# Kernel tuning notes

Measured on AMD Instinct MI355X. Metric: run time of the kernel, lower is better.

Reference implementation:

```python
import jax, jax.numpy as jnp
import numpy as np

I, H, M, C, LOC, K = 512, 256, 80, 1024, 32, 31
C2 = C // 2
B, S, T = 32, 256, 800


def setup_inputs() -> dict:
    key = jax.random.key(0)
    ks = jax.random.split(key, 20)
    sc = 0.02
    return {
        "encodings": jax.random.normal(ks[0], (B, S, I), jnp.float32),
        "queries": jax.random.normal(ks[1], (B, T, H), jnp.float32),
        "outputs": jax.random.normal(ks[2], (B, T, M), jnp.float32),
        "mask": jnp.ones((B, S), jnp.float32),
        # GRUCell (PyTorch layout: gates ordered r, z, n)
        "w_ih": jax.random.normal(ks[3], (3 * C, I + H), jnp.float32) * sc,
        "w_hh": jax.random.normal(ks[4], (3 * C, C), jnp.float32) * sc,
        "b_ih": jax.random.normal(ks[5], (3 * C,), jnp.float32) * sc,
        "b_hh": jax.random.normal(ks[6], (3 * C,), jnp.float32) * sc,
        "w_q": jax.random.normal(ks[7], (C2, C), jnp.float32) * sc,        # proj_query
        "w_loc1": jax.random.normal(ks[8], (LOC, 1, K), jnp.float32) * sc, # Conv1d(1, loc, K)
        "w_loc2": jax.random.normal(ks[9], (C2, LOC), jnp.float32) * sc,   # Conv1d(loc, C2, 1)
        "w_k": jax.random.normal(ks[10], (C2, I), jnp.float32) * sc,       # proj_key
        "b_k": jax.random.normal(ks[11], (C2,), jnp.float32) * sc,
        "w_agg": jax.random.normal(ks[12], (C2,), jnp.float32) * sc,       # Conv1d(C2, 1, 1)
        "w_t1": jax.random.normal(ks[13], (C, I + C + M), jnp.float32) * sc,
        "b_t1": jax.random.normal(ks[14], (C,), jnp.float32) * sc,
        "w_t2": jax.random.normal(ks[15], (C,), jnp.float32) * sc,
    }


def _conv1d(x, w, pad):
    # x: [B, Cin, S], w: [Cout, Cin, K]
    return jax.lax.conv_general_dilated(
        x, w, window_strides=(1,), padding=[(pad, pad)],
        dimension_numbers=("NCH", "OIH", "NCH"))


def _aligner(encodings, queries, outputs, maskb,
             w_ih, w_hh, b_ih, b_hh, w_q, w_loc1, w_loc2, w_k, b_k,
             w_agg, w_t1, b_t1, w_t2):
    bsize, seqlen, _ = encodings.shape
    # key projection: [B, S, C2]
    key = encodings @ w_k.T + b_k
    h0 = jnp.zeros((bsize, C), encodings.dtype)
    align0 = jnp.full((bsize, seqlen), 1.0 / seqlen, encodings.dtype)
    alpha0 = jnp.zeros((bsize, seqlen), encodings.dtype).at[:, 0].set(1.0)
    trans0 = jnp.full((bsize, 1), 0.5, encodings.dtype)

    def step(carry, xt):
        h, align, trans, alpha = carry
        query, frame = xt  # [B,H], [B,M]
        prev = jnp.einsum("bsi,bs->bi", encodings, alpha)
        x = jnp.concatenate([query, prev], axis=-1)  # [B, H+I]
        gx = x @ w_ih.T + b_ih
        gh = h @ w_hh.T + b_hh
        xr, xz, xn = jnp.split(gx, 3, axis=-1)
        hr, hz, hn = jnp.split(gh, 3, axis=-1)
        r = jax.nn.sigmoid(xr + hr)
        z = jax.nn.sigmoid(xz + hz)
        n = jnp.tanh(xn + r * hn)
        h_new = (1.0 - z) * n + z * h  # GRUCell update
        # location features: [B,1,S] -> [B,LOC,S] -> [B,C2,S]
        loc = _conv1d(align[:, None, :], w_loc1, K // 2)
        loc = jnp.einsum("cl,bls->bcs", w_loc2, loc)
        score = loc + (h_new @ w_q.T)[..., None] + key.swapaxes(1, 2)  # [B,C2,S]
        energy = jnp.einsum("c,bcs->bs", w_agg, jnp.tanh(score))
        energy = jnp.where(maskb, -jnp.inf, energy)
        align_new = jax.nn.softmax(energy, axis=-1)
        shifted = jnp.pad(alpha, ((0, 0), (1, 0)))[:, :-1]  # F.pad(alpha, [1,-1])
        alpha_new = ((1.0 - trans) * alpha + trans * shifted + 1e-7) * align_new
        alpha_new = alpha_new / alpha_new.sum(axis=-1, keepdims=True)
        attend = jnp.einsum("bsi,bs->bi", encodings, alpha_new)
        t_in = jnp.concatenate([attend, frame, h_new], axis=-1)
        t = jax.nn.sigmoid(jnp.tanh(t_in @ w_t1.T + b_t1) @ w_t2[:, None])  # [B,1]
        return (h_new, align_new, t, alpha_new), alpha_new

    xs = (queries.swapaxes(0, 1), outputs.swapaxes(0, 1))
    _, alphas = jax.lax.scan(step, (h0, align0, trans0, alpha0), xs)
    return alphas.swapaxes(0, 1)  # [B, T, S]


def reference(encodings, queries, outputs, mask,
              w_ih, w_hh, b_ih, b_hh, w_q, w_loc1, w_loc2, w_k, b_k,
              w_agg, w_t1, b_t1, w_t2):
    maskb = ~(mask.astype(bool))
    return _aligner(encodings, queries, outputs, maskb,
                    w_ih, w_hh, b_ih, b_hh, w_q, w_loc1, w_loc2, w_k, b_k,
                    w_agg, w_t1, b_t1, w_t2)
```

## Files before the change

### kernel.cpp

```cpp
#include <hip/hip_runtime.h>
#include <cstdint>
#include <cstddef>


namespace cfg {
constexpr int NB = 32, NS = 256, NI = 512, NHq = 256, NM = 80;
constexpr int NC = 1024, NC2 = 512, NT = 800;
constexpr int NBLK = 256, NTHR = 512;

constexpr size_t OFF_KEYT  = 0;
constexpr size_t OFF_WKT   = OFF_KEYT + (size_t)NB * NS * NC2;
constexpr size_t OFF_PU    = OFF_WKT + (size_t)NI * NC2;
constexpr size_t OFF_H     = OFF_PU + (size_t)2 * NB * NI;
constexpr size_t OFF_H16   = OFF_H + (size_t)2 * NC * NB;
constexpr size_t OFF_E     = OFF_H16 + (size_t)NB * NC;
constexpr size_t OFF_W     = OFF_E + (size_t)2 * NB * NS;
constexpr size_t OFF_SE    = OFF_W + (size_t)2 * NB * NS;
constexpr size_t OFF_SW    = OFF_SE + 64;
constexpr size_t OFF_TPART = OFF_SW + 64;
constexpr size_t OFF_TRED  = OFF_TPART + (size_t)NBLK * NB;
constexpr size_t OFF_QBUF  = OFF_TRED + 32;
constexpr size_t OFF_BAR   = OFF_QBUF + (size_t)NB * NC2;
constexpr size_t OFF_Q16   = OFF_BAR + 4608;
constexpr size_t OFF_F16   = OFF_Q16 + (size_t)NT * NB * NHq / 2;
constexpr size_t OFF_WQ16  = OFF_F16 + (size_t)NT * NB * 128 / 2;
constexpr size_t WS_FLOATS = OFF_WQ16 + (size_t)NC2 * NC / 2;
}
using namespace cfg;

typedef __attribute__((ext_vector_type(8))) short short8;
typedef __attribute__((ext_vector_type(4))) float f32x4;

#define MF(a, b, c) __builtin_amdgcn_mfma_f32_16x16x32_bf16((a), (b), (c), 0, 0, 0)
#define LDSC(d, p) asm volatile("global_load_dwordx4 %0, %1, off sc0 sc1" : "=v"(d) : "v"(p))

__device__ __forceinline__ float ld_cg(const float* p) {
  return __hip_atomic_load(p, __ATOMIC_RELAXED, __HIP_MEMORY_SCOPE_AGENT);
}
__device__ __forceinline__ void st_cg(float* p, float v) {
  __hip_atomic_store(p, v, __ATOMIC_RELAXED, __HIP_MEMORY_SCOPE_AGENT);
}
__device__ __forceinline__ void st_cg_u16(unsigned short* p, unsigned short v) {
  asm volatile("global_store_short %0, %1, off sc0 sc1" :: "v"(p), "v"((unsigned)v) : "memory");
}

__device__ __forceinline__ void vw7(short8& a0, short8& a1, short8& a2, short8& a3,
                                    short8& a4, short8& a5, short8& a6) {
  asm volatile("s_waitcnt vmcnt(0)"
               : "+v"(a0), "+v"(a1), "+v"(a2), "+v"(a3), "+v"(a4), "+v"(a5), "+v"(a6));
}
__device__ __forceinline__ void vw8(short8& a0, short8& a1, short8& a2, short8& a3,
                                    short8& a4, short8& a5, short8& a6, short8& a7) {
  asm volatile("s_waitcnt vmcnt(0)"
               : "+v"(a0), "+v"(a1), "+v"(a2), "+v"(a3), "+v"(a4), "+v"(a5), "+v"(a6), "+v"(a7));
}
__device__ __forceinline__ void vw10(short8& a0, short8& a1, short8& a2, short8& a3, short8& a4,
                                     short8& a5, short8& a6, short8& a7, short8& a8, short8& a9) {
  asm volatile("s_waitcnt vmcnt(0)"
               : "+v"(a0), "+v"(a1), "+v"(a2), "+v"(a3), "+v"(a4), "+v"(a5), "+v"(a6),
                 "+v"(a7), "+v"(a8), "+v"(a9));
}
__device__ __forceinline__ void vw15(short8& a0, short8& a1, short8& a2, short8& a3, short8& a4,
                                     short8& a5, short8& a6, short8& a7, short8& a8, short8& a9,
                                     short8& aa, short8& ab2, short8& ac, short8& ad, short8& ae) {
  asm volatile("s_waitcnt vmcnt(0)"
               : "+v"(a0), "+v"(a1), "+v"(a2), "+v"(a3), "+v"(a4), "+v"(a5), "+v"(a6),
                 "+v"(a7), "+v"(a8), "+v"(a9), "+v"(aa), "+v"(ab2), "+v"(ac), "+v"(ad), "+v"(ae));
}
__device__ __forceinline__ void vw16f(f32x4& a0, f32x4& a1, f32x4& a2, f32x4& a3, f32x4& a4,
                                      f32x4& a5, f32x4& a6, f32x4& a7, f32x4& b0, f32x4& b1,
                                      f32x4& b2, f32x4& b3, f32x4& b4, f32x4& b5, f32x4& b6,
                                      f32x4& b7) {
  asm volatile("s_waitcnt vmcnt(0)"
               : "+v"(a0), "+v"(a1), "+v"(a2), "+v"(a3), "+v"(a4), "+v"(a5), "+v"(a6), "+v"(a7),
                 "+v"(b0), "+v"(b1), "+v"(b2), "+v"(b3), "+v"(b4), "+v"(b5), "+v"(b6), "+v"(b7));
}

__device__ __forceinline__ float frcp(float x) {
#if __has_builtin(__builtin_amdgcn_rcpf)
  return __builtin_amdgcn_rcpf(x);
#else
  return 1.f / x;
#endif
}
__device__ __forceinline__ float fsig(float x) { return frcp(1.f + __expf(-x)); }
__device__ __forceinline__ float ftanh(float x) {
  const float e = __expf(2.f * x);
  return 1.f - 2.f * frcp(e + 1.f);
}
__device__ __forceinline__ short f2bf(float f) {
  unsigned u = __float_as_uint(f);
  u += 0x7FFFu + ((u >> 16) & 1u);
  return (short)(u >> 16);
}
__device__ __forceinline__ float bf2f(short s) {
  return __uint_as_float(((unsigned)(unsigned short)s) << 16);
}
__device__ __forceinline__ short8 cvt8(f32x4 lo, f32x4 hi) {
  short8 a;
  a[0] = f2bf(lo[0]); a[1] = f2bf(lo[1]); a[2] = f2bf(lo[2]); a[3] = f2bf(lo[3]);
  a[4] = f2bf(hi[0]); a[5] = f2bf(hi[1]); a[6] = f2bf(hi[2]); a[7] = f2bf(hi[3]);
  return a;
}

__device__ __forceinline__ void gbarrier(unsigned* root, unsigned* flags, unsigned& ph) {
  ++ph;
  asm volatile("s_waitcnt vmcnt(0)" ::: "memory");
  __syncthreads();
  if (blockIdx.x == 0) {
    const int t = threadIdx.x;
    if (t > 0 && t < 256) {
      while (__hip_atomic_load(&flags[t * 16], __ATOMIC_RELAXED, __HIP_MEMORY_SCOPE_AGENT) < ph)
        __builtin_amdgcn_s_sleep(1);
    }
    __syncthreads();
    if (t == 0)
      __hip_atomic_store(root, ph, __ATOMIC_RELAXED, __HIP_MEMORY_SCOPE_AGENT);
  } else {
    if (threadIdx.x == 0) {
      __hip_atomic_store(&flags[blockIdx.x * 16], ph, __ATOMIC_RELAXED, __HIP_MEMORY_SCOPE_AGENT);
      while (__hip_atomic_load(root, __ATOMIC_RELAXED, __HIP_MEMORY_SCOPE_AGENT) < ph)
        __builtin_amdgcn_s_sleep(1);
    }
  }
  __syncthreads();
}

__device__ __forceinline__ float wcat_val(const float* __restrict__ w_ih,
                                          const float* __restrict__ w_hh,
                                          const float* __restrict__ w_t1,
                                          int kind, int c, int k) {
  if (kind < 3) {
    const int gr = kind * NC + c;
    if (k < 768) return w_ih[(size_t)gr * 768 + k];
    if (k < 1792) return w_hh[(size_t)gr * NC + (k - 768)];
    return 0.f;
  }
  if (k >= 256 && k < 768) return w_t1[(size_t)c * 1616 + (k - 256)];
  if (k >= 768 && k < 1792) return w_t1[(size_t)c * 1616 + 592 + (k - 768)];
  if (k >= 1792 && k < 1872) return w_t1[(size_t)c * 1616 + 512 + (k - 1792)];
  return 0.f;
}

__global__ void k_init(const float* __restrict__ enc, const float* __restrict__ queries,
                       const float* __restrict__ outputs, const float* __restrict__ w_k,
                       const float* __restrict__ w_q, float* __restrict__ ws) {
  const size_t t0 = (size_t)blockIdx.x * blockDim.x + threadIdx.x;
  const size_t gs = (size_t)gridDim.x * blockDim.x;
  for (size_t x = t0; x < (size_t)NI * NC2; x += gs) {
    const int i = (int)(x / NC2), c2 = (int)(x % NC2);
    ws[OFF_WKT + x] = w_k[(size_t)c2 * NI + i];
  }
  for (size_t x = t0; x < (size_t)NB * NI; x += gs) {
    const int b = (int)(x / NI), i = (int)(x % NI);
    ws[OFF_PU + x] = 0.f;
    ws[OFF_PU + (size_t)NB * NI + b * NI + i] = enc[(size_t)b * NS * NI + i];
  }
  for (size_t x = t0; x < (size_t)2 * NC * NB; x += gs) ws[OFF_H + x] = 0.f;
  for (size_t x = t0; x < (size_t)NB * NC; x += gs) ws[OFF_H16 + x] = 0.f;
  for (size_t x = t0; x < (size_t)NB * NS; x += gs) {
    ws[OFF_E + x] = 0.f;
    ws[OFF_E + (size_t)NB * NS + x] = 1.f;
    ws[OFF_W + x] = 0.f;
    ws[OFF_W + (size_t)NB * NS + x] = ((x & (NS - 1)) == 0) ? 1.f : 0.f;
  }
  for (size_t x = t0; x < (size_t)NB; x += gs) {
    ws[OFF_SE + x] = 0.f; ws[OFF_SE + NB + x] = (float)NS;
    ws[OFF_SW + x] = 0.f; ws[OFF_SW + NB + x] = 1.f;
    ws[OFF_TRED + x] = 0.f;
  }
  unsigned* bar = (unsigned*)(ws + OFF_BAR);
  for (size_t x = t0; x < 4608; x += gs) bar[x] = 0u;
  unsigned short* Q16 = (unsigned short*)(ws + OFF_Q16);
  for (size_t x = t0; x < (size_t)NT * NB * NHq; x += gs) {
    const int k = (int)(x & (NHq - 1));
    const int b = (int)((x >> 8) & (NB - 1));
    const int t = (int)(x >> 13);
    Q16[x] = (unsigned short)f2bf(queries[((size_t)b * NT + t) * NHq + k]);
  }
  unsigned short* F16 = (unsigned short*)(ws + OFF_F16);
  for (size_t x = t0; x < (size_t)NT * NB * 128; x += gs) {
    const int k = (int)(x & 127);
    const int b = (int)((x >> 7) & (NB - 1));
    const int t = (int)(x >> 12);
    F16[x] = (k < NM) ? (unsigned short)f2bf(outputs[((size_t)b * NT + t) * NM + k]) : 0;
  }
  unsigned short* WQ16 = (unsigned short*)(ws + OFF_WQ16);
  for (size_t x = t0; x < (size_t)NC2 * NC; x += gs)
    WQ16[x] = (unsigned short)f2bf(w_q[x]);
}

__global__ __launch_bounds__(NTHR) void k_key(const float* __restrict__ enc,
                                              const float* __restrict__ b_k,
                                              float* __restrict__ ws) {
  __shared__ float encl[4 * NI];
  const int bid = blockIdx.x, tid = threadIdx.x;
  const int b = bid >> 3, s0 = (bid & 7) * 32;
  const float* wkT = ws + OFF_WKT;
  float* keyT = ws + OFF_KEYT;
  const float bk = b_k[tid];
  for (int q = 0; q < 8; ++q) {
    const int sb = s0 + q * 4;
    for (int x = tid; x < 4 * NI; x += NTHR) {
      const int ss = x >> 9, i = x & (NI - 1);
      encl[x] = enc[((size_t)(b * NS + sb + ss)) * NI + i];
    }
    __syncthreads();
    float a0 = bk, a1 = bk, a2 = bk, a3 = bk;
    for (int i = 0; i < NI; ++i) {
      const float wv = wkT[(size_t)i * NC2 + tid];
      a0 += wv * encl[i];           a1 += wv * encl[NI + i];
      a2 += wv * encl[2 * NI + i];  a3 += wv * encl[3 * NI + i];
    }
    keyT[((size_t)(b * NS + sb + 0)) * NC2 + tid] = a0;
    keyT[((size_t)(b * NS + sb + 1)) * NC2 + tid] = a1;
    keyT[((size_t)(b * NS + sb + 2)) * NC2 + tid] = a2;
    keyT[((size_t)(b * NS + sb + 3)) * NC2 + tid] = a3;
    __syncthreads();
  }
}

__global__ __launch_bounds__(NTHR, 2) void k_main(
    const float* __restrict__ enc, const float* __restrict__ mask,
    const float* __restrict__ w_ih, const float* __restrict__ w_hh,
    const float* __restrict__ b_ih, const float* __restrict__ b_hh,
    const float* __restrict__ w_loc1, const float* __restrict__ w_loc2,
    const float* __restrict__ w_agg, const float* __restrict__ w_t1,
    const float* __restrict__ b_t1, const float* __restrict__ w_t2,
    float* ws, float* __restrict__ out) {
  const int bid = blockIdx.x, tid = threadIdx.x;
  float* const keyT = ws + OFF_KEYT;
  float* const PU = ws + OFF_PU;
  float* const HB = ws + OFF_H;
  unsigned short* const HB16 = (unsigned short*)(ws + OFF_H16);
  float* const EB = ws + OFF_E;
  float* const WBUF = ws + OFF_W;
  float* const SEB = ws + OFF_SE;
  float* const SWB = ws + OFF_SW;
  float* const TPART = ws + OFF_TPART;
  float* const TRED = ws + OFF_TRED;
  float* const QBUF = ws + OFF_QBUF;
  unsigned* const root = (unsigned*)(ws + OFF_BAR);
  unsigned* const flags = root + 16;
  unsigned* const qflags = root + 4112;
  const unsigned short* const Q16 = (const unsigned short*)(ws + OFF_Q16);
  const unsigned short* const F16 = (const unsigned short*)(ws + OFF_F16);
  const unsigned short* const WQ16 = (const unsigned short*)(ws + OFF_WQ16);

  __shared__ float Cred[2 * 5 * 4 * 64];
  __shared__ float gout2[5 * 4 * 32];
  __shared__ float swinv_l[32];
  __shared__ float tredl[128];
  __shared__ float alignl[72];
  __shared__ float wl2[34];
  __shared__ float qbl[520];
  __shared__ float Epart[32 * 9];
  __shared__ float wstash[32];
  __shared__ float scal[4];

  const int lane = tid & 63, wv = tid >> 6;
  const int m2 = wv >> 2, k4 = wv & 3;
  const int kg = lane >> 4;
  const int ab = m2 * 16 + (lane & 15);
  const int cs = bid * 4;
  const int pb_b = bid >> 3, pb_s0 = (bid & 7) * 32;
  const int col = lane & 15, quad = lane >> 4;
  unsigned ph = 0;

  short8 wreg[16];
  {
    const int n = lane & 15;
    const int kind = n >> 2, ch = cs + (n & 3);
#pragma unroll
    for (int si = 0; si < 16; ++si) {
      int s = (k4 == 0) ? (si < 8 ? si : (si < 15 ? 16 + si : -1))
            : (k4 == 1) ? 8 + si
            : (k4 == 2) ? (si < 15 ? 31 + si : -1)
                        : (si < 14 ? 46 + si : -1);
      short8 w = {0, 0, 0, 0, 0, 0, 0, 0};
      if (s >= 0) {
        const int k0 = s * 32 + kg * 8;
#pragma unroll
        for (int jj = 0; jj < 8; ++jj)
          w[jj] = f2bf(wcat_val(w_ih, w_hh, w_t1, kind, ch, k0 + jj));
      }
      wreg[si] = w;
    }
  }
  short8 wcA[4];
  unsigned keylo[4][2], keyhi[4][2];
  f32x4 wagr[4];
#pragma unroll
  for (int t = 0; t < 4; ++t) {
    const int mt = 4 * wv + t;
    short8 wfr;
#pragma unroll
    for (int jj = 0; jj < 8; ++jj) {
      const int k = quad * 8 + jj;
      float s = 0.f;
      if (k < 31) {
        const int c2 = mt * 16 + col;
        for (int l = 0; l < 32; ++l) s += w_loc2[c2 * 32 + l] * w_loc1[l * 31 + k];
      }
      wfr[jj] = f2bf(s);
    }
    wcA[t] = wfr;
    const int c2r = mt * 16 + quad * 4;
#pragma unroll
    for (int r = 0; r < 4; ++r) wagr[t][r] = w_agg[c2r + r];
#pragma unroll
    for (int nt = 0; nt < 2; ++nt) {
      const float* kp = &keyT[((size_t)(pb_b * NS + pb_s0 + nt * 16 + col)) * NC2 + c2r];
      keylo[t][nt] = ((unsigned)(unsigned short)f2bf(kp[0])) |
                     (((unsigned)(unsigned short)f2bf(kp[1])) << 16);
      keyhi[t][nt] = ((unsigned)(unsigned short)f2bf(kp[2])) |
                     (((unsigned)(unsigned short)f2bf(kp[3])) << 16);
    }
  }
  if (tid >= 62 && tid < 72) alignl[tid] = 0.f;
  __syncthreads();

  for (int j = 0; j < NT; ++j) {
    const int p = j & 1;
    const float* pu_prev = PU + (size_t)(1 - p) * NB * NI;
    float* pu_cur = PU + (size_t)p * NB * NI;
    const float* h_prev = HB + (size_t)(1 - p) * NC * NB;
    float* h_cur = HB + (size_t)p * NC * NB;
    const unsigned short* hb16_prev = HB16 + (size_t)(1 - p) * NB * NC;
    unsigned short* hb16_cur = HB16 + (size_t)p * NB * NC;
    const float* e_prev = EB + (size_t)(1 - p) * NB * NS;
    float* e_cur = EB + (size_t)p * NB * NS;
    const float* w_prev = WBUF + (size_t)(1 - p) * NB * NS;
    float* w_cur = WBUF + (size_t)p * NB * NS;
    const float* se_prev = SEB + (size_t)(1 - p) * NB;
    float* se_cur = SEB + (size_t)p * NB;
    const float* sw_prev = SWB + (size_t)(1 - p) * NB;
    float* sw_cur = SWB + (size_t)p * NB;

    f32x4 bacc[2][4];

    if (tid < 64) st_cg(&pu_cur[bid * 64 + tid], 0.f);
    if (bid == 0 && tid < NB) st_cg(&se_cur[tid], 0.f);
    if (bid == 1 && tid < NB) st_cg(&sw_cur[tid], 0.f);
    if (tid < NB) swinv_l[tid] = 1.f / ld_cg(&sw_prev[tid]);
    if (tid == 0) scal[0] = ld_cg(&se_prev[pb_b]);
    if (tid < 62) {
      const int sp = pb_s0 + tid - 15;
      alignl[tid] = (sp >= 0 && sp < NS) ? ld_cg(&e_prev[pb_b * NS + sp]) : 0.f;
    }
    if (tid >= 64 && tid < 97) {
      const int i2 = tid - 64, sp = pb_s0 + i2 - 1;
      wl2[i2] = (sp >= 0 && sp < NS) ? ld_cg(&w_prev[pb_b * NS + sp]) : 0.f;
    }
    __syncthreads();

    if (j >= 1 && bid < NB && tid < NS)
      out[((size_t)bid * NT + (j - 1)) * NS + tid] = ld_cg(&w_prev[bid * NS + tid]) * swinv_l[bid];

    f32x4 accA = {0.f, 0.f, 0.f, 0.f}, accB = {0.f, 0.f, 0.f, 0.f};
    if (k4 == 0) {
      const unsigned short* qp = Q16 + ((size_t)j * NB + ab) * NHq + kg * 8;
      const unsigned short* hp = hb16_prev + (size_t)ab * NC + kg * 8;
      short8 h0, h1, h2, h3, h4, h5, h6;
      LDSC(h0, hp);        LDSC(h1, hp + 32);   LDSC(h2, hp + 64);  LDSC(h3, hp + 96);
      LDSC(h4, hp + 128);  LDSC(h5, hp + 160);  LDSC(h6, hp + 192);
      const short8 q0 = *(const short8*)(qp);
      const short8 q1 = *(const short8*)(qp + 32);
      const short8 q2 = *(const short8*)(qp + 64);
      const short8 q3 = *(const short8*)(qp + 96);
      const short8 q4 = *(const short8*)(qp + 128);
      const short8 q5 = *(const short8*)(qp + 160);
      const short8 q6 = *(const short8*)(qp + 192);
      const short8 q7 = *(const short8*)(qp + 224);
      vw7(h0, h1, h2, h3, h4, h5, h6);
      accA = MF(q0, wreg[0], accA); accA = MF(q1, wreg[1], accA);
      accA = MF(q2, wreg[2], accA); accA = MF(q3, wreg[3], accA);
      accA = MF(q4, wreg[4], accA); accA = MF(q5, wreg[5], accA);
      accA = MF(q6, wreg[6], accA); accA = MF(q7, wreg[7], accA);
      accB = MF(h0, wreg[8], accB);  accB = MF(h1, wreg[9], accB);
      accB = MF(h2, wreg[10], accB); accB = MF(h3, wreg[11], accB);
      accB = MF(h4, wreg[12], accB); accB = MF(h5, wreg[13], accB);
      accB = MF(h6, wreg[14], accB);
    } else if (k4 == 1) {
      const float* pp = pu_prev + (size_t)ab * NI + kg * 8;
#pragma unroll
      for (int rd = 0; rd < 2; ++rd) {
        const float* pb = pp + rd * 256;
        f32x4 a0, a1, a2, a3, a4, a5, a6, a7, b0, b1, b2, b3, b4, b5, b6, b7;
        LDSC(a0, pb);        LDSC(b0, pb + 4);
        LDSC(a1, pb + 32);   LDSC(b1, pb + 36);
        LDSC(a2, pb + 64);   LDSC(b2, pb + 68);
        LDSC(a3, pb + 96);   LDSC(b3, pb + 100);
        LDSC(a4, pb + 128);  LDSC(b4, pb + 132);
        LDSC(a5, pb + 160);  LDSC(b5, pb + 164);
        LDSC(a6, pb + 192);  LDSC(b6, pb + 196);
        LDSC(a7, pb + 224);  LDSC(b7, pb + 228);
        vw16f(a0, a1, a2, a3, a4, a5, a6, a7, b0, b1, b2, b3, b4, b5, b6, b7);
        const int w0 = rd * 8;
        accA = MF(cvt8(a0, b0), wreg[w0 + 0], accA);
        accA = MF(cvt8(a1, b1), wreg[w0 + 1], accA);
        accA = MF(cvt8(a2, b2), wreg[w0 + 2], accA);
        accA = MF(cvt8(a3, b3), wreg[w0 + 3], accA);
        accA = MF(cvt8(a4, b4), wreg[w0 + 4], accA);
        accA = MF(cvt8(a5, b5), wreg[w0 + 5], accA);
        accA = MF(cvt8(a6, b6), wreg[w0 + 6], accA);
        accA = MF(cvt8(a7, b7), wreg[w0 + 7], accA);
      }
    } else if (k4 == 2) {
      const unsigned short* hp = hb16_prev + (size_t)ab * NC + kg * 8 + 224;
      short8 h0, h1, h2, h3, h4, h5, h6, h7, h8, h9, ha, hb2, hc, hd, he;
      LDSC(h0, hp);        LDSC(h1, hp + 32);  LDSC(h2, hp + 64);  LDSC(h3, hp + 96);
      LDSC(h4, hp + 128);  LDSC(h5, hp + 160); LDSC(h6, hp + 192); LDSC(h7, hp + 224);
      LDSC(h8, hp + 256);  LDSC(h9, hp + 288); LDSC(ha, hp + 320); LDSC(hb2, hp + 352);
      LDSC(hc, hp + 384);  LDSC(hd, hp + 416); LDSC(he, hp + 448);
      vw15(h0, h1, h2, h3, h4, h5, h6, h7, h8, h9, ha, hb2, hc, hd, he);
      accA = MF(h0, wreg[0], accA);  accA = MF(h1, wreg[1], accA);
      accA = MF(h2, wreg[2], accA);  accA = MF(h3, wreg[3], accA);
      accA = MF(h4, wreg[4], accA);  accA = MF(h5, wreg[5], accA);
      accA = MF(h6, wreg[6], accA);  accA = MF(h7, wreg[7], accA);
      accA = MF(h8, wreg[8], accA);  accA = MF(h9, wreg[9], accA);
      accA = MF(ha, wreg[10], accA); accA = MF(hb2, wreg[11], accA);
      accA = MF(hc, wreg[12], accA); accA = MF(hd, wreg[13], accA);
      accA = MF(he, wreg[14], accA);
    } else {
      const unsigned short* hp = hb16_prev + (size_t)ab * NC + kg * 8 + 704;
      short8 h0, h1, h2, h3, h4, h5, h6, h7, h8, h9;
      LDSC(h0, hp);        LDSC(h1, hp + 32);  LDSC(h2, hp + 64);  LDSC(h3, hp + 96);
      LDSC(h4, hp + 128);  LDSC(h5, hp + 160); LDSC(h6, hp + 192); LDSC(h7, hp + 224);
      LDSC(h8, hp + 256);  LDSC(h9, hp + 288);
      short8 f0 = {0,0,0,0,0,0,0,0}, f1 = f0, f2 = f0, f3 = f0;
      if (j > 0) {
        const unsigned short* fp = F16 + ((size_t)(j - 1) * NB + ab) * 128 + kg * 8;
        f0 = *(const short8*)(fp);
        f1 = *(const short8*)(fp + 32);
        f2 = *(const short8*)(fp + 64);
        f3 = *(const short8*)(fp + 96);
      }
      vw10(h0, h1, h2, h3, h4, h5, h6, h7, h8, h9);
      accA = MF(h0, wreg[0], accA); accA = MF(h1, wreg[1], accA);
      accA = MF(h2, wreg[2], accA); accA = MF(h3, wreg[3], accA);
      accA = MF(h4, wreg[4], accA); accA = MF(h5, wreg[5], accA);
      accA = MF(h6, wreg[6], accA); accA = MF(h7, wreg[7], accA);
      accA = MF(h8, wreg[8], accA); accA = MF(h9, wreg[9], accA);
      accA = MF(f0, wreg[10], accA); accA = MF(f1, wreg[11], accA);
      accA = MF(f2, wreg[12], accA); accA = MF(f3, wreg[13], accA);
    }
    {
      auto cidx = [](int m, int sg, int r, int l) { return ((m * 5 + sg) * 4 + r) * 64 + l; };
      if (k4 == 0) {
#pragma unroll
        for (int r = 0; r < 4; ++r) {
          Cred[cidx(m2, 0, r, lane)] = accA[r];
          Cred[cidx(m2, 1, r, lane)] = accB[r];
        }
      } else {
        const int sg = 1 + k4;
#pragma unroll
        for (int r = 0; r < 4; ++r) Cred[cidx(m2, sg, r, lane)] = accA[r];
      }
    }
    {
      const float invSE = 1.f / scal[0];
#pragma unroll
      for (int nt = 0; nt < 2; ++nt) {
        const int base = nt * 16 + col + quad * 8;
        short8 bv;
#pragma unroll
        for (int jj = 0; jj < 8; ++jj) bv[jj] = f2bf(alignl[base + jj] * invSE);
#pragma unroll
        for (int t = 0; t < 4; ++t) {
          f32x4 acc;
          acc[0] = __uint_as_float(keylo[t][nt] << 16);
          acc[1] = __uint_as_float(keylo[t][nt] & 0xffff0000u);
          acc[2] = __uint_as_float(keyhi[t][nt] << 16);
          acc[3] = __uint_as_float(keyhi[t][nt] & 0xffff0000u);
          bacc[nt][t] = MF(wcA[t], bv, acc);
        }
      }
    }
    __syncthreads();
    {
      const int n = tid & 15, b = tid >> 4;
      const int m2r = b >> 4, bm = b & 15, l = (bm >> 2) * 16 + n, r = bm & 3;
      auto cidx = [](int m, int sg, int rr, int ll) { return ((m * 5 + sg) * 4 + rr) * 64 + ll; };
      const float s0 = Cred[cidx(m2r, 0, r, l)];
      const float sB = Cred[cidx(m2r, 1, r, l)];
      const float s1 = Cred[cidx(m2r, 2, r, l)];
      const float s2 = sB + Cred[cidx(m2r, 3, r, l)] + Cred[cidx(m2r, 4, r, l)];
      const float swv = swinv_l[b];
      const int kind = n >> 2, c4o = n & 3;
      if (kind == 2) {
        gout2[2 * 128 + c4o * 32 + b] = s0 + swv * s1;
        gout2[3 * 128 + c4o * 32 + b] = s2;
      } else {
        const int slot = (kind == 3) ? 4 : kind;
        gout2[slot * 128 + c4o * 32 + b] = s0 + swv * s1 + s2;
      }
    }
    __syncthreads();
    if (tid < 128) {
      const int c4o = tid >> 5, b = tid & 31, c = cs + c4o;
      const float xr = gout2[0 * 128 + c4o * 32 + b] + b_ih[c] + b_hh[c];
      const float xz = gout2[1 * 128 + c4o * 32 + b] + b_ih[NC + c] + b_hh[NC + c];
      const float xn = gout2[2 * 128 + c4o * 32 + b] + b_ih[2 * NC + c];
      const float hn = gout2[3 * 128 + c4o * 32 + b] + b_hh[2 * NC + c];
      const float tp = gout2[4 * 128 + c4o * 32 + b];
      const float r = fsig(xr), z = fsig(xz);
      const float nn = ftanh(xn + r * hn);
      const float hnew = (1.f - z) * nn + z * h_prev[c * 32 + b];
      h_cur[c * 32 + b] = hnew;
      st_cg_u16(&hb16_cur[(size_t)b * NC + c], (unsigned short)f2bf(hnew));
      tredl[c4o * 32 + b] = w_t2[c] * ftanh(tp + b_t1[c]);
    }
    __syncthreads();
    if (tid < NB)
      st_cg(&TPART[bid * NB + tid],
            tredl[tid] + tredl[32 + tid] + tredl[64 + tid] + tredl[96 + tid]);
    gbarrier(root, flags, ph);

    if (bid < 32) {
      f32x4 qacc = {0.f, 0.f, 0.f, 0.f};
      const unsigned short* hb = hb16_cur + (size_t)ab * NC + kg * 8;
      short8 g0, g1, g2, g3, g4, g5, g6, g7;
      LDSC(g0, hb + (k4 * 8 + 0) * 32); LDSC(g1, hb + (k4 * 8 + 1) * 32);
      LDSC(g2, hb + (k4 * 8 + 2) * 32); LDSC(g3, hb + (k4 * 8 + 3) * 32);
      LDSC(g4, hb + (k4 * 8 + 4) * 32); LDSC(g5, hb + (k4 * 8 + 5) * 32);
      LDSC(g6, hb + (k4 * 8 + 6) * 32); LDSC(g7, hb + (k4 * 8 + 7) * 32);
      const int jq = bid * 16 + col;
      const unsigned short* wp = WQ16 + (size_t)jq * NC + k4 * 8 * 32 + kg * 8;
      vw8(g0, g1, g2, g3, g4, g5, g6, g7);
      qacc = MF(g0, *(const short8*)(wp), qacc);
      qacc = MF(g1, *(const short8*)(wp + 32), qacc);
      qacc = MF(g2, *(const short8*)(wp + 64), qacc);
      qacc = MF(g3, *(const short8*)(wp + 96), qacc);
      qacc = MF(g4, *(const short8*)(wp + 128), qacc);
      qacc = MF(g5, *(const short8*)(wp + 160), qacc);
      qacc = MF(g6, *(const short8*)(wp + 192), qacc);
      qacc = MF(g7, *(const short8*)(wp + 224), qacc);
#pragma unroll
      for (int r = 0; r < 4; ++r) Cred[((m2 * 4 + k4) * 4 + r) * 64 + lane] = qacc[r];
      __syncthreads();
      {
        const int col2 = tid & 15, b2 = tid >> 4;
        const int m2r = b2 >> 4, bm = b2 & 15, l = (bm >> 2) * 16 + col2, r = bm & 3;
        float s = 0.f;
#pragma unroll
        for (int kk = 0; kk < 4; ++kk) s += Cred[((m2r * 4 + kk) * 4 + r) * 64 + l];
        st_cg(&QBUF[(size_t)b2 * NC2 + bid * 16 + col2], s);
      }
      asm volatile("s_waitcnt vmcnt(0)" ::: "memory");
      __syncthreads();
      if (tid == 0)
        __hip_atomic_store(&qflags[bid * 4], (unsigned)(j + 1),
                           __ATOMIC_RELAXED, __HIP_MEMORY_SCOPE_AGENT);
    } else if (bid >= 64 && bid < 96) {
      const int b2 = bid - 64;
      float v = (tid < NBLK) ? ld_cg(&TPART[tid * NB + b2]) : 0.f;
#pragma unroll
      for (int off = 32; off > 0; off >>= 1) v += __shfl_down(v, off);
      if (lane == 0) Cred[wv] = v;
      __syncthreads();
      if (tid == 0) {
        float s = 0.f;
#pragma unroll
        for (int w8 = 0; w8 < 8; ++w8) s += Cred[w8];
        st_cg(&TRED[b2], s);
        asm volatile("s_waitcnt vmcnt(0)" ::: "memory");
        __hip_atomic_store(&qflags[(32 + b2) * 4], (unsigned)(j + 1),
                           __ATOMIC_RELAXED, __HIP_MEMORY_SCOPE_AGENT);
      }
    }

    {
      const int b = pb_b, s0v = pb_s0;
      if (tid < 64) {
        const unsigned tgt = (unsigned)(j + 1);
        while (__hip_atomic_load(&qflags[tid * 4], __ATOMIC_RELAXED,
                                 __HIP_MEMORY_SCOPE_AGENT) < tgt)
          __builtin_amdgcn_s_sleep(2);
      }
      __syncthreads();
      qbl[tid] = ld_cg(&QBUF[(size_t)b * NC2 + tid]);
      if (tid == 0) scal[2] = ld_cg(&TRED[b]);
      __syncthreads();
      const float invSW = swinv_l[b];
      const float tr = (j == 0) ? 0.5f : fsig(scal[2]);
#pragma unroll
      for (int nt = 0; nt < 2; ++nt) {
        float pe = 0.f;
#pragma unroll
        for (int t = 0; t < 4; ++t) {
          const int c2b = (4 * wv + t) * 16 + quad * 4;
          const f32x4 av = bacc[nt][t];
          pe += wagr[t][0] * ftanh(av[0] + qbl[c2b + 0]);
          pe += wagr[t][1] * ftanh(av[1] + qbl[c2b + 1]);
          pe += wagr[t][2] * ftanh(av[2] + qbl[c2b + 2]);
          pe += wagr[t][3] * ftanh(av[3] + qbl[c2b + 3]);
        }
        pe += __shfl_xor(pe, 16);
        pe += __shfl_xor(pe, 32);
        if (lane < 16) Epart[(nt * 16 + col) * 9 + wv] = pe;
      }
      __syncthreads();
      if (tid < 32) {
        const int sl = tid, s = s0v + sl;
        float Ev = 0.f;
#pragma unroll
        for (int w8 = 0; w8 < 8; ++w8) Ev += Epart[sl * 9 + w8];
        const float ev = (mask[b * NS + s] != 0.f) ? __expf(Ev) : 0.f;
        const float csv = ((1.f - tr) * wl2[sl + 1] + tr * wl2[sl]) * invSW + 1e-7f;
        const float wvv = csv * ev;
        st_cg(&e_cur[b * NS + s], ev);
        st_cg(&w_cur[b * NS + s], wvv);
        wstash[sl] = wvv;
        float se = ev, sw2 = wvv;
#pragma unroll
        for (int off = 16; off > 0; off >>= 1) {
          se += __shfl_down(se, off, 32);
          sw2 += __shfl_down(sw2, off, 32);
        }
        if (sl == 0) { atomicAdd(&se_cur[b], se); atomicAdd(&sw_cur[b], sw2); }
      }
      __syncthreads();
      {
        float acc = 0.f;
        const float* encb = enc + ((size_t)(b * NS + s0v)) * NI + tid;
#pragma unroll 8
        for (int ss = 0; ss < 32; ++ss) acc += wstash[ss] * encb[(size_t)ss * NI];
        atomicAdd(&pu_cur[(size_t)b * NI + tid], acc);
      }
    }
    gbarrier(root, flags, ph);
  }

  if (bid < NB && tid < NS) {
    const float invSW = 1.f / ld_cg(&SWB[NB + bid]);
    out[((size_t)bid * NT + (NT - 1)) * NS + tid] =
        ld_cg(&WBUF[(size_t)NB * NS + bid * NS + tid]) * invSW;
  }
}

extern "C" void kernel_launch(void* const* d_in, const int* in_sizes, int n_in,
                              void* d_out, int out_size, void* d_ws, size_t ws_size,
                              hipStream_t stream) {
  const float* enc     = (const float*)d_in[0];
  const float* queries = (const float*)d_in[1];
  const float* outputs = (const float*)d_in[2];
  const float* mask    = (const float*)d_in[3];
  const float* w_ih    = (const float*)d_in[4];
  const float* w_hh    = (const float*)d_in[5];
  const float* b_ih    = (const float*)d_in[6];
  const float* b_hh    = (const float*)d_in[7];
  const float* w_q     = (const float*)d_in[8];
  const float* w_loc1  = (const float*)d_in[9];
  const float* w_loc2  = (const float*)d_in[10];
  const float* w_k     = (const float*)d_in[11];
  const float* b_k     = (const float*)d_in[12];
  const float* w_agg   = (const float*)d_in[13];
  const float* w_t1    = (const float*)d_in[14];
  const float* b_t1    = (const float*)d_in[15];
  const float* w_t2    = (const float*)d_in[16];
  float* ws = (float*)d_ws;
  float* out = (float*)d_out;
  (void)in_sizes; (void)n_in; (void)out_size; (void)ws_size;

  k_init<<<dim3(1024), dim3(256), 0, stream>>>(enc, queries, outputs, w_k, w_q, ws);
  k_key<<<dim3(NBLK), dim3(NTHR), 0, stream>>>(enc, b_k, ws);
  k_main<<<dim3(NBLK), dim3(NTHR), 0, stream>>>(enc, mask, w_ih, w_hh, b_ih, b_hh,
                                                w_loc1, w_loc2, w_agg, w_t1,
                                                b_t1, w_t2, ws, out);
}
```

Baseline: 22.37 ms.

## Restructure per-step sync: distributed T reduction, replicated barrier flags, bf16 encodings

The dedicated blocks that reduced the transition partials are removed. Every block now reads its batch row of the transposed TPART and reduces it locally. The global barrier root flag and the new query-ready signal are replicated across 32 cache-line-spaced slots to cut polling contention, with one block aggregating the q-flags and broadcasting them. The alignment-key MFMA is moved after the barrier so it overlaps the waiting, and the attend accumulation reads a bf16 copy of the encodings to halve that traffic. This adds extra TPART reads per block and lowers precision in the context vector.

```diff
diff --git a/kernel.cpp b/kernel.cpp
--- a/kernel.cpp
+++ b/kernel.cpp
@@ -18,13 +18,14 @@
 constexpr size_t OFF_SE    = OFF_W + (size_t)2 * NB * NS;
 constexpr size_t OFF_SW    = OFF_SE + 64;
 constexpr size_t OFF_TPART = OFF_SW + 64;
-constexpr size_t OFF_TRED  = OFF_TPART + (size_t)NBLK * NB;
+constexpr size_t OFF_TRED  = OFF_TPART + (size_t)NB * NBLK;
 constexpr size_t OFF_QBUF  = OFF_TRED + 32;
 constexpr size_t OFF_BAR   = OFF_QBUF + (size_t)NB * NC2;
-constexpr size_t OFF_Q16   = OFF_BAR + 4608;
+constexpr size_t OFF_Q16   = OFF_BAR + 8192;
 constexpr size_t OFF_F16   = OFF_Q16 + (size_t)NT * NB * NHq / 2;
 constexpr size_t OFF_WQ16  = OFF_F16 + (size_t)NT * NB * 128 / 2;
-constexpr size_t WS_FLOATS = OFF_WQ16 + (size_t)NC2 * NC / 2;
+constexpr size_t OFF_ENC16 = OFF_WQ16 + (size_t)NC2 * NC / 2;
+constexpr size_t WS_FLOATS = OFF_ENC16 + (size_t)NB * NS * NI / 2;
 }
 using namespace cfg;
 
@@ -93,8 +94,8 @@
   u += 0x7FFFu + ((u >> 16) & 1u);
   return (short)(u >> 16);
 }
-__device__ __forceinline__ float bf2f(short s) {
-  return __uint_as_float(((unsigned)(unsigned short)s) << 16);
+__device__ __forceinline__ float bfu(unsigned short u) {
+  return __uint_as_float(((unsigned)u) << 16);
 }
 __device__ __forceinline__ short8 cvt8(f32x4 lo, f32x4 hi) {
   short8 a;
@@ -107,6 +108,7 @@
   ++ph;
   asm volatile("s_waitcnt vmcnt(0)" ::: "memory");
   __syncthreads();
+  unsigned* rootrep = root + 4352;
   if (blockIdx.x == 0) {
     const int t = threadIdx.x;
     if (t > 0 && t < 256) {
@@ -114,12 +116,13 @@
         __builtin_amdgcn_s_sleep(1);
     }
     __syncthreads();
-    if (t == 0)
-      __hip_atomic_store(root, ph, __ATOMIC_RELAXED, __HIP_MEMORY_SCOPE_AGENT);
+    if (t < 32)
+      __hip_atomic_store(&rootrep[t * 16], ph, __ATOMIC_RELAXED, __HIP_MEMORY_SCOPE_AGENT);
   } else {
     if (threadIdx.x == 0) {
       __hip_atomic_store(&flags[blockIdx.x * 16], ph, __ATOMIC_RELAXED, __HIP_MEMORY_SCOPE_AGENT);
-      while (__hip_atomic_load(root, __ATOMIC_RELAXED, __HIP_MEMORY_SCOPE_AGENT) < ph)
+      while (__hip_atomic_load(&rootrep[(blockIdx.x & 31) * 16], __ATOMIC_RELAXED,
+                               __HIP_MEMORY_SCOPE_AGENT) < ph)
         __builtin_amdgcn_s_sleep(1);
     }
   }
@@ -169,8 +172,9 @@
     ws[OFF_SW + x] = 0.f; ws[OFF_SW + NB + x] = 1.f;
     ws[OFF_TRED + x] = 0.f;
   }
+  for (size_t x = t0; x < (size_t)NB * NBLK; x += gs) ws[OFF_TPART + x] = 0.f;
   unsigned* bar = (unsigned*)(ws + OFF_BAR);
-  for (size_t x = t0; x < 4608; x += gs) bar[x] = 0u;
+  for (size_t x = t0; x < 8192; x += gs) bar[x] = 0u;
   unsigned short* Q16 = (unsigned short*)(ws + OFF_Q16);
   for (size_t x = t0; x < (size_t)NT * NB * NHq; x += gs) {
     const int k = (int)(x & (NHq - 1));
@@ -188,6 +192,9 @@
   unsigned short* WQ16 = (unsigned short*)(ws + OFF_WQ16);
   for (size_t x = t0; x < (size_t)NC2 * NC; x += gs)
     WQ16[x] = (unsigned short)f2bf(w_q[x]);
+  unsigned short* ENC16 = (unsigned short*)(ws + OFF_ENC16);
+  for (size_t x = t0; x < (size_t)NB * NS * NI; x += gs)
+    ENC16[x] = (unsigned short)f2bf(enc[x]);
 }
 
 __global__ __launch_bounds__(NTHR) void k_key(const float* __restrict__ enc,
@@ -238,19 +245,21 @@
   float* const SEB = ws + OFF_SE;
   float* const SWB = ws + OFF_SW;
   float* const TPART = ws + OFF_TPART;
-  float* const TRED = ws + OFF_TRED;
   float* const QBUF = ws + OFF_QBUF;
   unsigned* const root = (unsigned*)(ws + OFF_BAR);
   unsigned* const flags = root + 16;
-  unsigned* const qflags = root + 4112;
+  unsigned* const qflag = root + 5120;
+  unsigned* const rootrep2 = root + 5632;
   const unsigned short* const Q16 = (const unsigned short*)(ws + OFF_Q16);
   const unsigned short* const F16 = (const unsigned short*)(ws + OFF_F16);
   const unsigned short* const WQ16 = (const unsigned short*)(ws + OFF_WQ16);
+  const unsigned short* const ENC16 = (const unsigned short*)(ws + OFF_ENC16);
 
   __shared__ float Cred[2 * 5 * 4 * 64];
   __shared__ float gout2[5 * 4 * 32];
   __shared__ float swinv_l[32];
   __shared__ float tredl[128];
+  __shared__ float redT[256];
   __shared__ float alignl[72];
   __shared__ float wl2[34];
   __shared__ float qbl[520];
@@ -336,8 +345,6 @@
     float* se_cur = SEB + (size_t)p * NB;
     const float* sw_prev = SWB + (size_t)(1 - p) * NB;
     float* sw_cur = SWB + (size_t)p * NB;
-
-    f32x4 bacc[2][4];
 
     if (tid < 64) st_cg(&pu_cur[bid * 64 + tid], 0.f);
     if (bid == 0 && tid < NB) st_cg(&se_cur[tid], 0.f);
@@ -459,25 +466,6 @@
         for (int r = 0; r < 4; ++r) Cred[cidx(m2, sg, r, lane)] = accA[r];
       }
     }
-    {
-      const float invSE = 1.f / scal[0];
-#pragma unroll
-      for (int nt = 0; nt < 2; ++nt) {
-        const int base = nt * 16 + col + quad * 8;
-        short8 bv;
-#pragma unroll
-        for (int jj = 0; jj < 8; ++jj) bv[jj] = f2bf(alignl[base + jj] * invSE);
-#pragma unroll
-        for (int t = 0; t < 4; ++t) {
-          f32x4 acc;
-          acc[0] = __uint_as_float(keylo[t][nt] << 16);
-          acc[1] = __uint_as_float(keylo[t][nt] & 0xffff0000u);
-          acc[2] = __uint_as_float(keyhi[t][nt] << 16);
-          acc[3] = __uint_as_float(keyhi[t][nt] & 0xffff0000u);
-          bacc[nt][t] = MF(wcA[t], bv, acc);
-        }
-      }
-    }
     __syncthreads();
     {
       const int n = tid & 15, b = tid >> 4;
@@ -514,9 +502,11 @@
     }
     __syncthreads();
     if (tid < NB)
-      st_cg(&TPART[bid * NB + tid],
+      st_cg(&TPART[(size_t)tid * NBLK + bid],
             tredl[tid] + tredl[32 + tid] + tredl[64 + tid] + tredl[96 + tid]);
     gbarrier(root, flags, ph);
+
+    const float tpv = (tid < 256) ? ld_cg(&TPART[(size_t)pb_b * NBLK + tid]) : 0.f;
 
     if (bid < 32) {
       f32x4 qacc = {0.f, 0.f, 0.f, 0.f};
@@ -551,37 +541,60 @@
       asm volatile("s_waitcnt vmcnt(0)" ::: "memory");
       __syncthreads();
       if (tid == 0)
-        __hip_atomic_store(&qflags[bid * 4], (unsigned)(j + 1),
+        __hip_atomic_store(&qflag[bid * 16], (unsigned)(j + 1),
                            __ATOMIC_RELAXED, __HIP_MEMORY_SCOPE_AGENT);
-    } else if (bid >= 64 && bid < 96) {
-      const int b2 = bid - 64;
-      float v = (tid < NBLK) ? ld_cg(&TPART[tid * NB + b2]) : 0.f;
-#pragma unroll
-      for (int off = 32; off > 0; off >>= 1) v += __shfl_down(v, off);
-      if (lane == 0) Cred[wv] = v;
+    }
+
+    if (tid < 256) redT[tid] = tpv;
+    __syncthreads();
+    if (tid < 64) {
+      float s = redT[tid] + redT[tid + 64] + redT[tid + 128] + redT[tid + 192];
+#pragma unroll
+      for (int off = 32; off > 0; off >>= 1) s += __shfl_xor(s, off);
+      if (tid == 0) scal[2] = s;
+    }
+    f32x4 bacc[2][4];
+    {
+      const float invSE = 1.f / scal[0];
+#pragma unroll
+      for (int nt = 0; nt < 2; ++nt) {
+        const int base = nt * 16 + col + quad * 8;
+        short8 bv;
+#pragma unroll
+        for (int jj = 0; jj < 8; ++jj) bv[jj] = f2bf(alignl[base + jj] * invSE);
+#pragma unroll
+        for (int t = 0; t < 4; ++t) {
+          f32x4 acc;
+          acc[0] = __uint_as_float(keylo[t][nt] << 16);
+          acc[1] = __uint_as_float(keylo[t][nt] & 0xffff0000u);
+          acc[2] = __uint_as_float(keyhi[t][nt] << 16);
+          acc[3] = __uint_as_float(keyhi[t][nt] & 0xffff0000u);
+          bacc[nt][t] = MF(wcA[t], bv, acc);
+        }
+      }
+    }
+    if (bid == 128) {
+      if (tid < 32) {
+        while (__hip_atomic_load(&qflag[tid * 16], __ATOMIC_RELAXED,
+                                 __HIP_MEMORY_SCOPE_AGENT) < (unsigned)(j + 1))
+          __builtin_amdgcn_s_sleep(1);
+      }
       __syncthreads();
+      if (tid < 32)
+        __hip_atomic_store(&rootrep2[tid * 16], (unsigned)(j + 1),
+                           __ATOMIC_RELAXED, __HIP_MEMORY_SCOPE_AGENT);
+    } else {
       if (tid == 0) {
-        float s = 0.f;
-#pragma unroll
-        for (int w8 = 0; w8 < 8; ++w8) s += Cred[w8];
-        st_cg(&TRED[b2], s);
-        asm volatile("s_waitcnt vmcnt(0)" ::: "memory");
-        __hip_atomic_store(&qflags[(32 + b2) * 4], (unsigned)(j + 1),
-                           __ATOMIC_RELAXED, __HIP_MEMORY_SCOPE_AGENT);
-      }
-    }
+        while (__hip_atomic_load(&rootrep2[(bid & 31) * 16], __ATOMIC_RELAXED,
+                                 __HIP_MEMORY_SCOPE_AGENT) < (unsigned)(j + 1))
+          __builtin_amdgcn_s_sleep(1);
+      }
+    }
+    __syncthreads();
 
     {
       const int b = pb_b, s0v = pb_s0;
-      if (tid < 64) {
-        const unsigned tgt = (unsigned)(j + 1);
-        while (__hip_atomic_load(&qflags[tid * 4], __ATOMIC_RELAXED,
-                                 __HIP_MEMORY_SCOPE_AGENT) < tgt)
-          __builtin_amdgcn_s_sleep(2);
-      }
-      __syncthreads();
       qbl[tid] = ld_cg(&QBUF[(size_t)b * NC2 + tid]);
-      if (tid == 0) scal[2] = ld_cg(&TRED[b]);
       __syncthreads();
       const float invSW = swinv_l[b];
       const float tr = (j == 0) ? 0.5f : fsig(scal[2]);
@@ -623,10 +636,10 @@
       }
       __syncthreads();
       {
+        const unsigned short* ep = ENC16 + ((size_t)(b * NS + s0v)) * NI + tid;
         float acc = 0.f;
-        const float* encb = enc + ((size_t)(b * NS + s0v)) * NI + tid;
 #pragma unroll 8
-        for (int ss = 0; ss < 32; ++ss) acc += wstash[ss] * encb[(size_t)ss * NI];
+        for (int ss = 0; ss < 32; ++ss) acc += wstash[ss] * bfu(ep[(size_t)ss * NI]);
         atomicAdd(&pu_cur[(size_t)b * NI + tid], acc);
       }
     }
```

New measurement: 20.34 ms. 9.0% less time.
